# Optimization experiments

Measured on AMD Instinct MI355X. Metric: run time of the kernel, lower is better.

## Reference

```python
import jax, jax.numpy as jnp
import numpy as np
import math

B, S, E, H, DK = 2, 2048, 1024, 16, 64  # batch, seq, embed, heads, d_k (= n_wires)

def setup_inputs() -> dict:
    key = jax.random.key(0)
    k1, k2, k3, k4, k5 = jax.random.split(key, 5)
    scale = 0.02
    return {
        "x": jax.random.normal(k1, (B, S, E), dtype=jnp.float32),
        "Wk": jax.random.normal(k2, (E, E), dtype=jnp.float32) * scale,
        "Wv": jax.random.normal(k3, (E, E), dtype=jnp.float32) * scale,
        "Wq": jax.random.normal(k4, (H, DK, E), dtype=jnp.float32) * scale,
        "theta": jax.random.normal(k5, (DK,), dtype=jnp.float32) * scale,
    }

def reference(x, Wk, Wv, Wq, theta):
    batch, seq, embed = x.shape
    n_heads, d_k = Wq.shape[0], Wq.shape[1]
    # K, V projections (nn.Linear, no bias): x @ W.T
    k = (x @ Wk.T).reshape(batch, seq, n_heads, d_k).transpose(0, 2, 1, 3)  # [B,H,S,dk]
    v = (x @ Wv.T).reshape(batch, seq, n_heads, d_k).transpose(0, 2, 1, 3)  # [B,H,S,dk]
    # Quantum query path: per-head linear proj -> RX(proj_i) then RX(theta_i) on wire i from |0>,
    # MeasureAll(PauliZ) on independent wires gives <Z_i> = cos(proj_i + theta_i) exactly.
    proj = jnp.einsum('bse,hde->bhsd', x, Wq)          # [B,H,S,dk]
    q = jnp.cos(proj + theta)                           # [B,H,S,dk]
    scores = jnp.einsum('bhsd,bhtd->bhst', q, k) / math.sqrt(d_k)  # [B,H,S,S]
    attn = jax.nn.softmax(scores, axis=-1)
    out = jnp.einsum('bhst,bhtd->bhsd', attn, v)        # [B,H,S,dk]
    return out.transpose(0, 2, 1, 3).reshape(batch, seq, embed)
```

## Files before the change

kernel.cpp:

```cpp
#include <hip/hip_runtime.h>
#include <hip/hip_bf16.h>

constexpr int B  = 2;
constexpr int S  = 2048;
constexpr int E  = 1024;
constexpr int H  = 16;
constexpr int DK = 64;
constexpr int M  = B * S;
constexpr int N3 = 3 * E;
constexpr long RSZ = (long)B * H * S * DK;

#define QSCALE 0.18033688011112042f

using bf16x8 = __attribute__((ext_vector_type(8))) __bf16;
using bf16x4 = __attribute__((ext_vector_type(4))) __bf16;
using f32x4  = __attribute__((ext_vector_type(4))) float;

__device__ __forceinline__ void async16(__bf16* lds, const __bf16* g) {
    __builtin_amdgcn_global_load_lds(
        (const __attribute__((address_space(1))) void*)g,
        (__attribute__((address_space(3))) void*)lds, 16, 0, 0);
}

__global__ __launch_bounds__(256)
void cvt_kernel(const float* __restrict__ x, const float* __restrict__ Wk,
                const float* __restrict__ Wv, const float* __restrict__ Wq,
                __bf16* __restrict__ xb, __bf16* __restrict__ wall) {
    const long e = ((long)blockIdx.x * 256 + threadIdx.x) * 4;
    const float* src;
    __bf16* dst;
    if (e < (long)M * E) { src = x + e; dst = xb + e; }
    else {
        const long e2 = e - (long)M * E;
        const int which = (int)(e2 >> 20);
        const long off  = e2 & ((1L << 20) - 1);
        src = (which == 0 ? Wk : which == 1 ? Wv : Wq) + off;
        dst = wall + e2;
    }
    float4 f = *reinterpret_cast<const float4*>(src);
    bf16x4 o;
    o[0] = (__bf16)f.x; o[1] = (__bf16)f.y; o[2] = (__bf16)f.z; o[3] = (__bf16)f.w;
    *reinterpret_cast<bf16x4*>(dst) = o;
}

__global__ __launch_bounds__(256, 3)
void qkv_gemm(const __bf16* __restrict__ xb, const __bf16* __restrict__ wall,
              const float* __restrict__ theta, __bf16* __restrict__ kvq) {
    __shared__ __align__(1024) __bf16 smem[6 * 128 * 32];
    __bf16* tile = smem;

    const int t    = threadIdx.x;
    const int lane = t & 63;
    const int w    = t >> 6;
    const int quad = lane >> 4;
    const int l16  = lane & 15;
    const int wm   = w >> 1, wn = w & 1;
    const int mbase = blockIdx.y * 128;
    const int nbase = blockIdx.x * 128;

    f32x4 acc[4][4];
    #pragma unroll
    for (int i = 0; i < 4; i++)
        #pragma unroll
        for (int j = 0; j < 4; j++)
            acc[i][j] = f32x4{0.f, 0.f, 0.f, 0.f};

    const int srow = lane >> 2;
    const int srcc = (lane & 3) ^ ((lane >> 3) & 3);
    const __bf16* ga = xb   + (long)(mbase + srow) * E + srcc * 8;
    const __bf16* gb = wall + (long)(nbase + srow) * E + srcc * 8;

    const int csw = (l16 >> 1) & 3;

    #pragma unroll
    for (int pt = 0; pt < 2; pt++) {
        #pragma unroll
        for (int c = 0; c < 2; c++) {
            async16(smem + pt * 4096 +         (c * 64 + w * 16) * 32,
                    ga + (long)(c * 64 + w * 16) * E + pt * 32);
            async16(smem + pt * 4096 + 12288 + (c * 64 + w * 16) * 32,
                    gb + (long)(c * 64 + w * 16) * E + pt * 32);
        }
    }

    int cur = 0;
    constexpr int ITERS = E / 32;
    for (int it = 0; it < ITERS; it++) {
        if (it < ITERS - 1) asm volatile("s_waitcnt vmcnt(4)" ::: "memory");
        else                asm volatile("s_waitcnt vmcnt(0)" ::: "memory");
        asm volatile("s_barrier" ::: "memory");

        if (it + 2 < ITERS) {
            const int pb  = (cur == 0) ? 2 : cur - 1;
            const int kk2 = (it + 2) * 32;
            #pragma unroll
            for (int c = 0; c < 2; c++) {
                async16(smem + pb * 4096 +         (c * 64 + w * 16) * 32,
                        ga + (long)(c * 64 + w * 16) * E + kk2);
                async16(smem + pb * 4096 + 12288 + (c * 64 + w * 16) * 32,
                        gb + (long)(c * 64 + w * 16) * E + kk2);
            }
        }

        const __bf16* Asb = smem + cur * 4096;
        const __bf16* Bsb = smem + cur * 4096 + 12288;
        bf16x8 a[4], b[4];
        #pragma unroll
        for (int i = 0; i < 4; i++)
            a[i] = *reinterpret_cast<const bf16x8*>(
                &Asb[(wm * 64 + i * 16 + l16) * 32 + (quad ^ csw) * 8]);
        #pragma unroll
        for (int j = 0; j < 4; j++)
            b[j] = *reinterpret_cast<const bf16x8*>(
                &Bsb[(wn * 64 + j * 16 + l16) * 32 + (quad ^ csw) * 8]);
        #pragma unroll
        for (int i = 0; i < 4; i++)
            #pragma unroll
            for (int j = 0; j < 4; j++)
                acc[i][j] = __builtin_amdgcn_mfma_f32_16x16x32_bf16(a[i], b[j], acc[i][j], 0, 0, 0);

        cur = (cur == 2) ? 0 : cur + 1;
    }

    const int region = nbase >> 10;
    const int bb = mbase >> 11;
    if (region == 1) {
        __syncthreads();
        #pragma unroll
        for (int i = 0; i < 4; i++) {
            const int cchunk = wm * 8 + i * 2 + (quad >> 1);
            #pragma unroll
            for (int j = 0; j < 4; j++) {
                const int cirb = wn * 64 + j * 16 + l16;
                const int cs = cchunk ^ l16;
                bf16x4 pk;
                #pragma unroll
                for (int r = 0; r < 4; r++) pk[r] = (__bf16)acc[i][j][r];
                *reinterpret_cast<bf16x4*>(&tile[cirb * 128 + cs * 8 + (quad & 1) * 4]) = pk;
            }
        }
        __syncthreads();
        const int h0 = (nbase & 1023) >> 6;
        __bf16* vt = kvq + RSZ;
        #pragma unroll
        for (int p = 0; p < 8; p++) {
            const int dcol = p * 16 + (t >> 4);
            const int lc = t & 15;
            const int cs2 = lc ^ (dcol & 15);
            bf16x8 vv = *reinterpret_cast<const bf16x8*>(&tile[dcol * 128 + cs2 * 8]);
            const int hh = h0 + (dcol >> 6), d = dcol & 63;
            *reinterpret_cast<bf16x8*>(
                &vt[((long)(bb * H + hh) * DK + d) * S + (mbase & 2047) + lc * 8]) = vv;
        }
    } else {
        __bf16* dst = kvq + (region == 2 ? 2 * RSZ : 0);
        float th[4];
        if (region == 2) {
            #pragma unroll
            for (int j = 0; j < 4; j++) th[j] = theta[j * 16 + l16];
        }
        #pragma unroll
        for (int i = 0; i < 4; i++) {
            const int row0 = mbase + wm * 64 + i * 16 + quad * 4;
            #pragma unroll
            for (int j = 0; j < 4; j++) {
                const int cir = (nbase & 1023) + wn * 64 + j * 16 + l16;
                const int h = cir >> 6, d = cir & 63;
                #pragma unroll
                for (int r = 0; r < 4; r++) {
                    const int s = (row0 + r) & 2047;
                    float v = acc[i][j][r];
                    if (region == 2) v = cosf(v + th[j]) * QSCALE;
                    dst[((long)(bb * H + h) * S + s) * DK + d] = (__bf16)v;
                }
            }
        }
    }
}

__global__ __launch_bounds__(256, 2)
void attn_kernel(const __bf16* __restrict__ q_ws, const __bf16* __restrict__ k_ws,
                 const __bf16* __restrict__ v_ws, float* __restrict__ out) {
    __shared__ __align__(1024) __bf16 Ks[2][64 * 64];
    __shared__ __align__(1024) __bf16 Vs[3][64 * 64];
    __shared__ __align__(16)   __bf16 Pl[4][2][32 * 72];
    __shared__ __align__(16)   float  ls_lds[4][32];

    const int lane = threadIdx.x & 63;
    const int w    = threadIdx.x >> 6;
    const int quad = lane >> 4;
    const int l16  = lane & 15;

    const int id    = blockIdx.x;
    const int bh    = (id & 7) + 8 * ((id >> 3) & 3);
    const int qbase = (id >> 5) * 128 + w * 32;

    const __bf16* qp = q_ws + (long)bh * S * DK;
    const __bf16* kp = k_ws + (long)bh * S * DK;
    const __bf16* vp = v_ws + (long)bh * DK * S;

    const int sr  = lane >> 3;
    const int scs = (lane & 7) ^ sr;

    bf16x8 bq[2][2];
    #pragma unroll
    for (int nt = 0; nt < 2; nt++)
        #pragma unroll
        for (int ks = 0; ks < 2; ks++)
            bq[nt][ks] = *reinterpret_cast<const bf16x8*>(
                qp + (long)(qbase + nt * 16 + l16) * DK + ks * 32 + quad * 8);

    f32x4 o[2][4];
    #pragma unroll
    for (int i = 0; i < 2; i++)
        #pragma unroll
        for (int j = 0; j < 4; j++) o[i][j] = f32x4{0.f, 0.f, 0.f, 0.f};
    float lsum[2] = {0.f, 0.f};

    auto pv_step = [&](const __bf16* Vsrc, const __bf16* Psrc) {
        #pragma unroll
        for (int kh = 0; kh < 2; kh++) {
            bf16x8 bv[4];
            #pragma unroll
            for (int nt = 0; nt < 4; nt++)
                bv[nt] = *reinterpret_cast<const bf16x8*>(
                    &Vsrc[(nt * 16 + l16) * 64 + ((kh * 4 + quad) ^ (l16 & 7)) * 8]);
            #pragma unroll
            for (int mt = 0; mt < 2; mt++) {
                bf16x8 ap = *reinterpret_cast<const bf16x8*>(
                    &Psrc[(mt * 16 + l16) * 72 + kh * 32 + quad * 8]);
                #pragma unroll
                for (int nt = 0; nt < 4; nt++)
                    o[mt][nt] = __builtin_amdgcn_mfma_f32_16x16x32_bf16(
                        ap, bv[nt], o[mt][nt], 0, 0, 0);
            }
        }
    };

    #pragma unroll
    for (int i = 0; i < 2; i++) {
        const int row = w * 16 + i * 8;
        async16(&Ks[0][row * 64], kp + (long)(row + sr) * DK + scs * 8);
        async16(&Vs[0][row * 64], vp + (long)(row + sr) * S + scs * 8);
    }

    int kcur = 0, vcur = 0, pcur = 0;
    constexpr int ITERS = S / 64;
    for (int it = 0; it < ITERS; it++) {
        asm volatile("s_waitcnt vmcnt(0)" ::: "memory");
        asm volatile("s_barrier" ::: "memory");

        const int vprv = (vcur == 0) ? 2 : vcur - 1;

        if (it + 1 < ITERS) {
            const int kt1  = (it + 1) * 64;
            const int vnxt = (vcur == 2) ? 0 : vcur + 1;
            #pragma unroll
            for (int i = 0; i < 2; i++) {
                const int row = w * 16 + i * 8;
                async16(&Ks[kcur ^ 1][row * 64], kp + (long)(kt1 + row + sr) * DK + scs * 8);
                async16(&Vs[vnxt][row * 64], vp + (long)(row + sr) * S + kt1 + scs * 8);
            }
        }

        f32x4 sacc[4][2];
        #pragma unroll
        for (int i = 0; i < 4; i++)
            #pragma unroll
            for (int j = 0; j < 2; j++) sacc[i][j] = f32x4{0.f, 0.f, 0.f, 0.f};
        #pragma unroll
        for (int ks = 0; ks < 2; ks++) {
            bf16x8 ak[4];
            #pragma unroll
            for (int mt = 0; mt < 4; mt++)
                ak[mt] = *reinterpret_cast<const bf16x8*>(
                    &Ks[kcur][(mt * 16 + l16) * 64 + ((ks * 4 + quad) ^ (l16 & 7)) * 8]);
            #pragma unroll
            for (int mt = 0; mt < 4; mt++)
                #pragma unroll
                for (int nt = 0; nt < 2; nt++)
                    sacc[mt][nt] = __builtin_amdgcn_mfma_f32_16x16x32_bf16(
                        ak[mt], bq[nt][ks], sacc[mt][nt], 0, 0, 0);
        }

        if (it) pv_step(&Vs[vprv][0], &Pl[w][pcur ^ 1][0]);

        #pragma unroll
        for (int mt = 0; mt < 4; mt++)
            #pragma unroll
            for (int nt = 0; nt < 2; nt++) {
                float p0 = __builtin_amdgcn_exp2f(sacc[mt][nt][0]);
                float p1 = __builtin_amdgcn_exp2f(sacc[mt][nt][1]);
                float p2 = __builtin_amdgcn_exp2f(sacc[mt][nt][2]);
                float p3 = __builtin_amdgcn_exp2f(sacc[mt][nt][3]);
                lsum[nt] += (p0 + p1) + (p2 + p3);
                bf16x4 pk;
                pk[0] = (__bf16)p0; pk[1] = (__bf16)p1;
                pk[2] = (__bf16)p2; pk[3] = (__bf16)p3;
                *reinterpret_cast<bf16x4*>(
                    &Pl[w][pcur][(nt * 16 + l16) * 72 + mt * 16 + quad * 4]) = pk;
            }

        kcur ^= 1;
        pcur ^= 1;
        vcur = (vcur == 2) ? 0 : vcur + 1;
    }

    {
        const int vprv = (vcur == 0) ? 2 : vcur - 1;
        pv_step(&Vs[vprv][0], &Pl[w][pcur ^ 1][0]);
    }

    #pragma unroll
    for (int nt = 0; nt < 2; nt++) {
        float v = lsum[nt];
        v += __shfl_xor(v, 16);
        v += __shfl_xor(v, 32);
        ls_lds[w][nt * 16 + l16] = v;
    }

    const int b = bh >> 4, h = bh & 15;
    #pragma unroll
    for (int mt = 0; mt < 2; mt++) {
        f32x4 lv = *reinterpret_cast<const f32x4*>(&ls_lds[w][mt * 16 + quad * 4]);
        #pragma unroll
        for (int r = 0; r < 4; r++) {
            const float inv = 1.0f / lv[r];
            const int srow = qbase + mt * 16 + quad * 4 + r;
            #pragma unroll
            for (int nt = 0; nt < 4; nt++)
                out[(long)(b * S + srow) * E + h * DK + nt * 16 + l16] = o[mt][nt][r] * inv;
        }
    }
}

__device__ inline bf16x8 cvt_frag(const float* __restrict__ p) {
    float4 f0 = *reinterpret_cast<const float4*>(p);
    float4 f1 = *reinterpret_cast<const float4*>(p + 4);
    bf16x8 r;
    r[0] = (__bf16)f0.x; r[1] = (__bf16)f0.y; r[2] = (__bf16)f0.z; r[3] = (__bf16)f0.w;
    r[4] = (__bf16)f1.x; r[5] = (__bf16)f1.y; r[6] = (__bf16)f1.z; r[7] = (__bf16)f1.w;
    return r;
}
template <int MODE>
__global__ __launch_bounds__(256, 2)
void proj_kernel(const float* __restrict__ x, const float* __restrict__ W,
                 const float* __restrict__ theta, __bf16* __restrict__ out) {
    const int lane = threadIdx.x & 63;
    const int w    = threadIdx.x >> 6;
    const int quad = lane >> 4;
    const int l16  = lane & 15;
    const int mbase = blockIdx.y * 128 + w * 32;
    const int nbase = blockIdx.x * 128;
    f32x4 acc[2][8];
    #pragma unroll
    for (int i = 0; i < 2; i++)
        #pragma unroll
        for (int j = 0; j < 8; j++) acc[i][j] = f32x4{0.f, 0.f, 0.f, 0.f};
    float th[4];
    if (MODE == 2) {
        #pragma unroll
        for (int j = 0; j < 4; j++) th[j] = theta[j * 16 + l16];
    }
    for (int kk = 0; kk < E; kk += 32) {
        bf16x8 a[2], b[8];
        #pragma unroll
        for (int mt = 0; mt < 2; mt++)
            a[mt] = cvt_frag(x + (long)(mbase + mt * 16 + l16) * E + kk + quad * 8);
        #pragma unroll
        for (int nt = 0; nt < 8; nt++)
            b[nt] = cvt_frag(W + (long)(nbase + nt * 16 + l16) * E + kk + quad * 8);
        #pragma unroll
        for (int mt = 0; mt < 2; mt++)
            #pragma unroll
            for (int nt = 0; nt < 8; nt++)
                acc[mt][nt] = __builtin_amdgcn_mfma_f32_16x16x32_bf16(a[mt], b[nt], acc[mt][nt], 0, 0, 0);
    }
    #pragma unroll
    for (int mt = 0; mt < 2; mt++) {
        const int row0 = mbase + mt * 16 + quad * 4;
        #pragma unroll
        for (int nt = 0; nt < 8; nt++) {
            const int col = nbase + nt * 16 + l16;
            const int h = col >> 6, d = col & 63;
            #pragma unroll
            for (int r = 0; r < 4; r++) {
                const int row = row0 + r;
                const int bb = row >> 11, s = row & 2047;
                float v = acc[mt][nt][r];
                if (MODE == 2) v = cosf(v + th[nt & 3]) * QSCALE;
                long idx;
                if (MODE == 1) idx = ((long)(bb * H + h) * DK + d) * S + s;
                else           idx = ((long)(bb * H + h) * S + s) * DK + d;
                out[idx] = (__bf16)v;
            }
        }
    }
}

extern "C" void kernel_launch(void* const* d_in, const int* in_sizes, int n_in,
                              void* d_out, int out_size, void* d_ws, size_t ws_size,
                              hipStream_t stream) {
    const float* x     = (const float*)d_in[0];
    const float* Wk    = (const float*)d_in[1];
    const float* Wv    = (const float*)d_in[2];
    const float* Wq    = (const float*)d_in[3];
    const float* theta = (const float*)d_in[4];
    float* out = (float*)d_out;

    __bf16* kvq  = (__bf16*)d_ws;
    __bf16* xb   = kvq + 3 * RSZ;
    __bf16* wall = xb + (long)M * E;
    __bf16* k_ws = kvq;
    __bf16* v_t  = kvq + RSZ;
    __bf16* q_ws = kvq + 2 * RSZ;

    const size_t need = (3 * RSZ + (long)M * E + (long)N3 * E) * 2;
    dim3 blk(256);
    if (ws_size >= need) {
        cvt_kernel<<<dim3(7168), blk, 0, stream>>>(x, Wk, Wv, Wq, xb, wall);
        qkv_gemm<<<dim3(N3 / 128, M / 128), blk, 0, stream>>>(xb, wall, theta, kvq);
    } else {
        dim3 gp(E / 128, M / 128);
        proj_kernel<0><<<gp, blk, 0, stream>>>(x, Wk, nullptr, k_ws);
        proj_kernel<1><<<gp, blk, 0, stream>>>(x, Wv, nullptr, v_t);
        proj_kernel<2><<<gp, blk, 0, stream>>>(x, Wq, theta, q_ws);
    }

    attn_kernel<<<dim3(512), blk, 0, stream>>>(q_ws, k_ws, v_t, out);
}
```

Measured before the change: 170.8 us.

## Shrink attention query tile to 16 rows per wave and drop PV pipelining

After: 191.8 us. 12.3% more time.

```diff
diff --git a/kernel.cpp b/kernel.cpp
--- a/kernel.cpp
+++ b/kernel.cpp
@@ -178,13 +178,13 @@
     }
 }
 
-__global__ __launch_bounds__(256, 2)
+__global__ __launch_bounds__(256, 3)
 void attn_kernel(const __bf16* __restrict__ q_ws, const __bf16* __restrict__ k_ws,
                  const __bf16* __restrict__ v_ws, float* __restrict__ out) {
     __shared__ __align__(1024) __bf16 Ks[2][64 * 64];
-    __shared__ __align__(1024) __bf16 Vs[3][64 * 64];
-    __shared__ __align__(16)   __bf16 Pl[4][2][32 * 72];
-    __shared__ __align__(16)   float  ls_lds[4][32];
+    __shared__ __align__(1024) __bf16 Vs[2][64 * 64];
+    __shared__ __align__(16)   __bf16 Pl[4][16 * 72];
+    __shared__ __align__(16)   float  ls_lds[4][16];
 
     const int lane = threadIdx.x & 63;
     const int w    = threadIdx.x >> 6;
@@ -193,7 +193,7 @@
 
     const int id    = blockIdx.x;
     const int bh    = (id & 7) + 8 * ((id >> 3) & 3);
-    const int qbase = (id >> 5) * 128 + w * 32;
+    const int qbase = (id >> 5) * 64 + w * 16;
 
     const __bf16* qp = q_ws + (long)bh * S * DK;
     const __bf16* kp = k_ws + (long)bh * S * DK;
@@ -202,40 +202,16 @@
     const int sr  = lane >> 3;
     const int scs = (lane & 7) ^ sr;
 
-    bf16x8 bq[2][2];
-    #pragma unroll
-    for (int nt = 0; nt < 2; nt++)
-        #pragma unroll
-        for (int ks = 0; ks < 2; ks++)
-            bq[nt][ks] = *reinterpret_cast<const bf16x8*>(
-                qp + (long)(qbase + nt * 16 + l16) * DK + ks * 32 + quad * 8);
-
-    f32x4 o[2][4];
-    #pragma unroll
-    for (int i = 0; i < 2; i++)
-        #pragma unroll
-        for (int j = 0; j < 4; j++) o[i][j] = f32x4{0.f, 0.f, 0.f, 0.f};
-    float lsum[2] = {0.f, 0.f};
-
-    auto pv_step = [&](const __bf16* Vsrc, const __bf16* Psrc) {
-        #pragma unroll
-        for (int kh = 0; kh < 2; kh++) {
-            bf16x8 bv[4];
-            #pragma unroll
-            for (int nt = 0; nt < 4; nt++)
-                bv[nt] = *reinterpret_cast<const bf16x8*>(
-                    &Vsrc[(nt * 16 + l16) * 64 + ((kh * 4 + quad) ^ (l16 & 7)) * 8]);
-            #pragma unroll
-            for (int mt = 0; mt < 2; mt++) {
-                bf16x8 ap = *reinterpret_cast<const bf16x8*>(
-                    &Psrc[(mt * 16 + l16) * 72 + kh * 32 + quad * 8]);
-                #pragma unroll
-                for (int nt = 0; nt < 4; nt++)
-                    o[mt][nt] = __builtin_amdgcn_mfma_f32_16x16x32_bf16(
-                        ap, bv[nt], o[mt][nt], 0, 0, 0);
-            }
-        }
-    };
+    bf16x8 bq[2];
+    #pragma unroll
+    for (int ks = 0; ks < 2; ks++)
+        bq[ks] = *reinterpret_cast<const bf16x8*>(
+            qp + (long)(qbase + l16) * DK + ks * 32 + quad * 8);
+
+    f32x4 o[4];
+    #pragma unroll
+    for (int j = 0; j < 4; j++) o[j] = f32x4{0.f, 0.f, 0.f, 0.f};
+    float lsum = 0.f;
 
     #pragma unroll
     for (int i = 0; i < 2; i++) {
@@ -244,93 +220,82 @@
         async16(&Vs[0][row * 64], vp + (long)(row + sr) * S + scs * 8);
     }
 
-    int kcur = 0, vcur = 0, pcur = 0;
+    int cur = 0;
     constexpr int ITERS = S / 64;
     for (int it = 0; it < ITERS; it++) {
         asm volatile("s_waitcnt vmcnt(0)" ::: "memory");
         asm volatile("s_barrier" ::: "memory");
 
-        const int vprv = (vcur == 0) ? 2 : vcur - 1;
-
         if (it + 1 < ITERS) {
-            const int kt1  = (it + 1) * 64;
-            const int vnxt = (vcur == 2) ? 0 : vcur + 1;
+            const int kt1 = (it + 1) * 64;
             #pragma unroll
             for (int i = 0; i < 2; i++) {
                 const int row = w * 16 + i * 8;
-                async16(&Ks[kcur ^ 1][row * 64], kp + (long)(kt1 + row + sr) * DK + scs * 8);
-                async16(&Vs[vnxt][row * 64], vp + (long)(row + sr) * S + kt1 + scs * 8);
-            }
-        }
-
-        f32x4 sacc[4][2];
-        #pragma unroll
-        for (int i = 0; i < 4; i++)
-            #pragma unroll
-            for (int j = 0; j < 2; j++) sacc[i][j] = f32x4{0.f, 0.f, 0.f, 0.f};
+                async16(&Ks[cur ^ 1][row * 64], kp + (long)(kt1 + row + sr) * DK + scs * 8);
+                async16(&Vs[cur ^ 1][row * 64], vp + (long)(row + sr) * S + kt1 + scs * 8);
+            }
+        }
+
+        f32x4 sacc[4];
+        #pragma unroll
+        for (int i = 0; i < 4; i++) sacc[i] = f32x4{0.f, 0.f, 0.f, 0.f};
         #pragma unroll
         for (int ks = 0; ks < 2; ks++) {
-            bf16x8 ak[4];
-            #pragma unroll
-            for (int mt = 0; mt < 4; mt++)
-                ak[mt] = *reinterpret_cast<const bf16x8*>(
-                    &Ks[kcur][(mt * 16 + l16) * 64 + ((ks * 4 + quad) ^ (l16 & 7)) * 8]);
-            #pragma unroll
-            for (int mt = 0; mt < 4; mt++)
-                #pragma unroll
-                for (int nt = 0; nt < 2; nt++)
-                    sacc[mt][nt] = __builtin_amdgcn_mfma_f32_16x16x32_bf16(
-                        ak[mt], bq[nt][ks], sacc[mt][nt], 0, 0, 0);
-        }
-
-        if (it) pv_step(&Vs[vprv][0], &Pl[w][pcur ^ 1][0]);
-
-        #pragma unroll
-        for (int mt = 0; mt < 4; mt++)
-            #pragma unroll
-            for (int nt = 0; nt < 2; nt++) {
-                float p0 = __builtin_amdgcn_exp2f(sacc[mt][nt][0]);
-                float p1 = __builtin_amdgcn_exp2f(sacc[mt][nt][1]);
-                float p2 = __builtin_amdgcn_exp2f(sacc[mt][nt][2]);
-                float p3 = __builtin_amdgcn_exp2f(sacc[mt][nt][3]);
-                lsum[nt] += (p0 + p1) + (p2 + p3);
-                bf16x4 pk;
-                pk[0] = (__bf16)p0; pk[1] = (__bf16)p1;
-                pk[2] = (__bf16)p2; pk[3] = (__bf16)p3;
-                *reinterpret_cast<bf16x4*>(
-                    &Pl[w][pcur][(nt * 16 + l16) * 72 + mt * 16 + quad * 4]) = pk;
-            }
-
-        kcur ^= 1;
-        pcur ^= 1;
-        vcur = (vcur == 2) ? 0 : vcur + 1;
+            #pragma unroll
+            for (int mt = 0; mt < 4; mt++) {
+                bf16x8 ak = *reinterpret_cast<const bf16x8*>(
+                    &Ks[cur][(mt * 16 + l16) * 64 + ((ks * 4 + quad) ^ (l16 & 7)) * 8]);
+                sacc[mt] = __builtin_amdgcn_mfma_f32_16x16x32_bf16(
+                    ak, bq[ks], sacc[mt], 0, 0, 0);
+            }
+        }
+
+        #pragma unroll
+        for (int mt = 0; mt < 4; mt++) {
+            float p0 = __builtin_amdgcn_exp2f(sacc[mt][0]);
+            float p1 = __builtin_amdgcn_exp2f(sacc[mt][1]);
+            float p2 = __builtin_amdgcn_exp2f(sacc[mt][2]);
+            float p3 = __builtin_amdgcn_exp2f(sacc[mt][3]);
+            lsum += (p0 + p1) + (p2 + p3);
+            bf16x4 pk;
+            pk[0] = (__bf16)p0; pk[1] = (__bf16)p1;
+            pk[2] = (__bf16)p2; pk[3] = (__bf16)p3;
+            *reinterpret_cast<bf16x4*>(
+                &Pl[w][l16 * 72 + mt * 16 + quad * 4]) = pk;
+        }
+
+        #pragma unroll
+        for (int kh = 0; kh < 2; kh++) {
+            bf16x8 ap = *reinterpret_cast<const bf16x8*>(
+                &Pl[w][l16 * 72 + kh * 32 + quad * 8]);
+            #pragma unroll
+            for (int nt = 0; nt < 4; nt++) {
+                bf16x8 bv = *reinterpret_cast<const bf16x8*>(
+                    &Vs[cur][(nt * 16 + l16) * 64 + ((kh * 4 + quad) ^ (l16 & 7)) * 8]);
+                o[nt] = __builtin_amdgcn_mfma_f32_16x16x32_bf16(
+                    ap, bv, o[nt], 0, 0, 0);
+            }
+        }
+
+        cur ^= 1;
     }
 
     {
-        const int vprv = (vcur == 0) ? 2 : vcur - 1;
-        pv_step(&Vs[vprv][0], &Pl[w][pcur ^ 1][0]);
-    }
-
-    #pragma unroll
-    for (int nt = 0; nt < 2; nt++) {
-        float v = lsum[nt];
+        float v = lsum;
         v += __shfl_xor(v, 16);
         v += __shfl_xor(v, 32);
-        ls_lds[w][nt * 16 + l16] = v;
+        ls_lds[w][l16] = v;
     }
 
     const int b = bh >> 4, h = bh & 15;
-    #pragma unroll
-    for (int mt = 0; mt < 2; mt++) {
-        f32x4 lv = *reinterpret_cast<const f32x4*>(&ls_lds[w][mt * 16 + quad * 4]);
-        #pragma unroll
-        for (int r = 0; r < 4; r++) {
-            const float inv = 1.0f / lv[r];
-            const int srow = qbase + mt * 16 + quad * 4 + r;
-            #pragma unroll
-            for (int nt = 0; nt < 4; nt++)
-                out[(long)(b * S + srow) * E + h * DK + nt * 16 + l16] = o[mt][nt][r] * inv;
-        }
+    f32x4 lv = *reinterpret_cast<const f32x4*>(&ls_lds[w][quad * 4]);
+    #pragma unroll
+    for (int r = 0; r < 4; r++) {
+        const float inv = 1.0f / lv[r];
+        const int srow = qbase + quad * 4 + r;
+        #pragma unroll
+        for (int nt = 0; nt < 4; nt++)
+            out[(long)(b * S + srow) * E + h * DK + nt * 16 + l16] = o[nt][r] * inv;
     }
 }
 
@@ -427,5 +392,5 @@
         proj_kernel<2><<<gp, blk, 0, stream>>>(x, Wq, theta, q_ws);
     }
 
-    attn_kernel<<<dim3(512), blk, 0, stream>>>(q_ws, k_ws, v_t, out);
-}
+    attn_kernel<<<dim3(1024), blk, 0, stream>>>(q_ws, k_ws, v_t, out);
+}
```
